# Optimization experiments

Measured on AMD Instinct MI355X. Metric: run time of the kernel, lower is better.

Reference implementation:

```python
import jax, jax.numpy as jnp
import numpy as np

NUM_SRC = 100000  # block src nodes
NUM_DST = 50000   # block dst nodes (first NUM_DST of src in DGL convention)
E = 800000        # edges, avg in-degree 16
D = 128           # in_dim == out_dim


def setup_inputs() -> dict:
    key = jax.random.key(0)
    k0, k1, k2, k3, k4 = jax.random.split(key, 5)
    h = jax.random.normal(k0, (NUM_SRC, D), dtype=jnp.float32)
    src = jax.random.randint(k1, (E,), 0, NUM_SRC)
    dst = jax.random.randint(k2, (E,), 0, NUM_DST)
    # GraphConv params: weight (in_dim, out_dim), bias (out_dim,)
    W = jax.random.normal(k3, (D, D), dtype=jnp.float32) / np.float32(np.sqrt(D))
    b = jnp.zeros((D,), dtype=jnp.float32)
    # gene_attn: Linear(out_dim, 1, bias=False)
    w_attn = jax.random.normal(k4, (D, 1), dtype=jnp.float32) / np.float32(np.sqrt(D))
    return {"h": h, "src": src, "dst": dst, "W": W, "b": b, "w_attn": w_attn}


def reference(h, src, dst, W, b, w_attn):
    ones = jnp.ones(src.shape, dtype=h.dtype)
    # DGL GraphConv norm='both': scale by out-degree(src)^-1/2 and in-degree(dst)^-1/2,
    # degrees clamped to min 1 (allow_zero_in_degree=True).
    deg_src = jax.ops.segment_sum(ones, src, num_segments=NUM_SRC)
    deg_dst = jax.ops.segment_sum(ones, dst, num_segments=NUM_DST)
    h_src = h * jax.lax.rsqrt(jnp.maximum(deg_src, 1.0))[:, None]
    # gather neighbor feats [E, D] then scatter-sum into dst nodes
    agg = jax.ops.segment_sum(h_src[src], dst, num_segments=NUM_DST)
    agg = agg * jax.lax.rsqrt(jnp.maximum(deg_dst, 1.0))[:, None]
    # in_dim == out_dim -> aggregate-then-weight (DGL order)
    out = agg @ W + b  # h[:num_dst] equivalent: agg is already dst-sized
    alpha = jax.nn.sigmoid(out @ w_attn)  # [NUM_DST, 1]
    return out * alpha, alpha
```

## Files before the change

kernel.cpp:

```cpp
#include <hip/hip_runtime.h>
#include <hip/hip_bf16.h>
#include <math.h>

#define DD 128
#define MAXDEG 64
#define BKT 64
#define SBKT 16
#define NB_MAX 1024
#define P_CH 8192
#define HBINS 16384
#define HBLK  32
#define HTHR  1024

using bf16x8 = __attribute__((ext_vector_type(8))) short;
using f32x4  = __attribute__((ext_vector_type(4))) float;

struct alignas(16) bfq { __hip_bfloat162 q[4]; };

__device__ inline float bf2f(short s) {
    unsigned int u = ((unsigned int)(unsigned short)s) << 16;
    float f;
    __builtin_memcpy(&f, &u, 4);
    return f;
}

__global__ __launch_bounds__(1024) void k1_kernel(
        const int* __restrict__ src, const int* __restrict__ dst,
        unsigned int* __restrict__ parts, unsigned int* __restrict__ bucket_cnt,
        int E, int NB, int nHist) {
    __shared__ unsigned int smem[HBINS];
    int t = threadIdx.x;
    int bid = blockIdx.x;
    if (bid < nHist) {
        int pass = bid / HBLK;
        int blk  = bid % HBLK;
        int lo   = pass * HBINS;
        for (int i = t; i < HBINS; i += 1024) smem[i] = 0;
        __syncthreads();
        int chunk = (E + HBLK - 1) / HBLK;
        int c0 = blk * chunk;
        int c1 = c0 + chunk; if (c1 > E) c1 = E;
        for (int i = c0 + t; i < c1; i += 1024) {
            unsigned int u = (unsigned int)(src[i] - lo);
            if (u < HBINS) atomicAdd(&smem[u], 1u);
        }
        __syncthreads();
        unsigned int* dstp = parts + ((size_t)bid << 14);
        for (int i = t; i < HBINS; i += 1024) dstp[i] = smem[i];
    } else {
        int b2 = bid - nHist;
        for (int b = t; b < NB; b += 1024) smem[b] = 0;
        __syncthreads();
        int c0 = b2 * P_CH;
        int c1 = c0 + P_CH; if (c1 > E) c1 = E;
        for (int i = c0 + t; i < c1; i += 1024)
            atomicAdd(&smem[dst[i] >> 6], 1u);
        __syncthreads();
        for (int b = t; b < NB; b += 1024)
            if (smem[b]) atomicAdd(&bucket_cnt[b], smem[b]);
    }
}

__global__ __launch_bounds__(256) void k2_kernel(
        const unsigned int* __restrict__ parts, unsigned int* __restrict__ deg_src,
        int num_src, const unsigned int* __restrict__ bucket_cnt,
        unsigned int* __restrict__ bucket_base, unsigned int* __restrict__ bucket_cur,
        int NB, int nMerge) {
    int bid = blockIdx.x;
    if (bid < nMerge) {
        int g = bid * 256 + threadIdx.x;
        if (g >= num_src) return;
        int pass = g >> 14;
        int r = g & (HBINS - 1);
        const unsigned int* p = parts + ((size_t)(pass * HBLK) << 14) + r;
        unsigned int s = 0;
#pragma unroll
        for (int b = 0; b < HBLK; ++b) s += p[(size_t)b << 14];
        deg_src[g] = s;
    } else {
        int lane = threadIdx.x;
        if (lane >= 64) return;
        unsigned int carry = 0;
        for (int b0 = 0; b0 < NB; b0 += 64) {
            int i = b0 + lane;
            unsigned int v = (i < NB) ? bucket_cnt[i] : 0u;
            unsigned int incl = v;
#pragma unroll
            for (int off = 1; off < 64; off <<= 1) {
                unsigned int u = __shfl_up(incl, off);
                if (lane >= off) incl += u;
            }
            unsigned int excl = incl - v + carry;
            if (i < NB) { bucket_base[i] = excl; bucket_cur[i] = excl; }
            carry += __shfl(incl, 63);
        }
        if (lane == 0) bucket_base[NB] = carry;
    }
}

__global__ __launch_bounds__(1024) void k3_kernel(
        const float* __restrict__ h, const unsigned int* __restrict__ deg_src,
        __hip_bfloat16* __restrict__ hb, const float* __restrict__ Wm,
        __hip_bfloat16* __restrict__ Wt, const int* __restrict__ src,
        const int* __restrict__ dst, unsigned int* __restrict__ bucket_cur,
        unsigned int* __restrict__ eparts, int E, int NB, int num_src,
        int nConv, int nWt) {
    __shared__ unsigned int smem[15360];
    int t = threadIdx.x;
    int bid = blockIdx.x;
    if (bid < nConv) {
        int idx = bid * 1024 + t;
        int total = num_src * (DD / 8);
        if (idx >= total) return;
        int row = idx >> 4;
        int c0  = (idx & 15) * 8;
        float nrm = rsqrtf(fmaxf((float)deg_src[row], 1.0f));
        const float4* p = reinterpret_cast<const float4*>(h + (size_t)row * DD + c0);
        float4 a = p[0], b = p[1];
        bfq o;
        o.q[0] = __float22bfloat162_rn(make_float2(a.x * nrm, a.y * nrm));
        o.q[1] = __float22bfloat162_rn(make_float2(a.z * nrm, a.w * nrm));
        o.q[2] = __float22bfloat162_rn(make_float2(b.x * nrm, b.y * nrm));
        o.q[3] = __float22bfloat162_rn(make_float2(b.z * nrm, b.w * nrm));
        *reinterpret_cast<bfq*>(hb + (size_t)row * DD + c0) = o;
    } else if (bid < nConv + nWt) {
        int idx = (bid - nConv) * 1024 + t;
        if (idx < DD * DD) {
            int c = idx >> 7, k = idx & 127;
            Wt[idx] = __float2bfloat16(Wm[k * DD + c]);
        }
    } else {
        int b2 = bid - nConv - nWt;
        unsigned int*   stage_s = smem;
        unsigned short* stage_d = (unsigned short*)(smem + 8192);
        unsigned int*   lhist   = smem + 12288;
        unsigned int*   lbase   = smem + 13312;
        unsigned int*   gbase   = smem + 14336;
        for (int b = t; b < NB_MAX; b += 1024) lhist[b] = 0;
        __syncthreads();
        int c0 = b2 * P_CH;
        int cnt = E - c0; if (cnt > P_CH) cnt = P_CH;
        int dreg[8], sreg[8];
#pragma unroll
        for (int k = 0; k < 8; ++k) {
            int j = t + k * 1024;
            if (j < cnt) {
                dreg[k] = dst[c0 + j];
                sreg[k] = src[c0 + j];
                atomicAdd(&lhist[dreg[k] >> 6], 1u);
            }
        }
        __syncthreads();
        int wid = t >> 6, lane = t & 63;
        unsigned int v = lhist[t];
        unsigned int x = v;
#pragma unroll
        for (int off = 1; off < 64; off <<= 1) {
            unsigned int u = __shfl_up(x, off);
            if (lane >= off) x += u;
        }
        if (lane == 63) gbase[wid] = x;
        __syncthreads();
        if (t < 16) {
            unsigned int w = gbase[t];
            unsigned int y = w;
#pragma unroll
            for (int off = 1; off < 16; off <<= 1) {
                unsigned int u = __shfl_up(y, off);
                if (t >= off) y += u;
            }
            gbase[t] = y - w;
        }
        __syncthreads();
        unsigned int excl = x - v + gbase[wid];
        __syncthreads();
        lbase[t] = excl;
        if (t < NB) {
            unsigned int c = lhist[t];
            gbase[t] = c ? atomicAdd(&bucket_cur[t], c) : 0u;
            lhist[t] = 0u;
        }
        __syncthreads();
#pragma unroll
        for (int k = 0; k < 8; ++k) {
            int j = t + k * 1024;
            if (j < cnt) {
                int bin = dreg[k] >> 6;
                unsigned int pos = lbase[bin] + atomicAdd(&lhist[bin], 1u);
                stage_d[pos] = (unsigned short)dreg[k];
                stage_s[pos] = (unsigned int)sreg[k];
            }
        }
        __syncthreads();
        for (int idx = t; idx < cnt; idx += 1024) {
            unsigned int d = stage_d[idx];
            unsigned int bin = d >> 6;
            unsigned int pos = gbase[bin] + ((unsigned int)idx - lbase[bin]);
            eparts[pos] = ((d & 63u) << 24) | stage_s[idx];
        }
    }
}

__global__ __launch_bounds__(256) void bgather_mfma_kernel(
        const __hip_bfloat16* __restrict__ hb,
        const unsigned int* __restrict__ eparts,
        const unsigned int* __restrict__ bucket_base,
        const __hip_bfloat16* __restrict__ Wt,
        const float* __restrict__ bias, const float* __restrict__ w_attn,
        float* __restrict__ out, float* __restrict__ alpha_out, int num_dst) {
    __shared__ unsigned int lcsr[SBKT * MAXDEG];
    __shared__ unsigned int cur[SBKT];
    __shared__ __hip_bfloat16 sagg[SBKT * DD];
    int t = threadIdx.x, wid = t >> 6, lane = t & 63;
    int b = blockIdx.x >> 2;
    unsigned int quarter = blockIdx.x & 3;
    if (t < SBKT) cur[t] = 0;
    __syncthreads();
    unsigned int e0 = bucket_base[b], e1 = bucket_base[b + 1];
    for (unsigned int i = e0 + t; i < e1; i += 256) {
        unsigned int e = eparts[i];
        unsigned int dlow = e >> 24;
        if ((dlow >> 4) == quarter) {
            unsigned int pos = atomicAdd(&cur[dlow & 15], 1u);
            if (pos < MAXDEG) lcsr[(dlow & 15) * MAXDEG + pos] = e & 0xFFFFFFu;
        }
    }
    __syncthreads();

    const bf16x8* hb8 = reinterpret_cast<const bf16x8*>(hb);
    char* sb = (char*)sagg;
    int g  = lane >> 4;
    int gl = lane & 15;
    {
        int r = wid * 4 + g;
        unsigned int degu = cur[r];
        int deg = (int)degu; if (deg > MAXDEG) deg = MAXDEG;
        const unsigned int* crow = &lcsr[r * MAXDEG];
        float acc[8];
#pragma unroll
        for (int j = 0; j < 8; ++j) acc[j] = 0.f;
        int i = 0;
        for (; i + 8 <= deg; i += 8) {
            uint4 qa = *reinterpret_cast<const uint4*>(crow + i);
            uint4 qb = *reinterpret_cast<const uint4*>(crow + i + 4);
            bf16x8 v0 = hb8[(size_t)qa.x * 16 + gl];
            bf16x8 v1 = hb8[(size_t)qa.y * 16 + gl];
            bf16x8 v2 = hb8[(size_t)qa.z * 16 + gl];
            bf16x8 v3 = hb8[(size_t)qa.w * 16 + gl];
            bf16x8 v4 = hb8[(size_t)qb.x * 16 + gl];
            bf16x8 v5 = hb8[(size_t)qb.y * 16 + gl];
            bf16x8 v6 = hb8[(size_t)qb.z * 16 + gl];
            bf16x8 v7 = hb8[(size_t)qb.w * 16 + gl];
#pragma unroll
            for (int j = 0; j < 8; ++j)
                acc[j] += ((bf2f(v0[j]) + bf2f(v1[j])) + (bf2f(v2[j]) + bf2f(v3[j])))
                        + ((bf2f(v4[j]) + bf2f(v5[j])) + (bf2f(v6[j]) + bf2f(v7[j])));
        }
        for (; i + 4 <= deg; i += 4) {
            uint4 q = *reinterpret_cast<const uint4*>(crow + i);
            bf16x8 v0 = hb8[(size_t)q.x * 16 + gl];
            bf16x8 v1 = hb8[(size_t)q.y * 16 + gl];
            bf16x8 v2 = hb8[(size_t)q.z * 16 + gl];
            bf16x8 v3 = hb8[(size_t)q.w * 16 + gl];
#pragma unroll
            for (int j = 0; j < 8; ++j)
                acc[j] += (bf2f(v0[j]) + bf2f(v1[j])) + (bf2f(v2[j]) + bf2f(v3[j]));
        }
        for (; i < deg; ++i) {
            bf16x8 v = hb8[(size_t)crow[i] * 16 + gl];
#pragma unroll
            for (int j = 0; j < 8; ++j) acc[j] += bf2f(v[j]);
        }
        float scd = rsqrtf(fmaxf((float)degu, 1.0f));
        bfq o;
#pragma unroll
        for (int j = 0; j < 4; ++j)
            o.q[j] = __float22bfloat162_rn(
                make_float2(acc[2 * j] * scd, acc[2 * j + 1] * scd));
        int byte = r * 256 + gl * 16;
        *reinterpret_cast<bfq*>(sb + (byte ^ ((r & 7) << 4))) = o;
    }
    __syncthreads();

    if (wid == 0) {
        int col = lane & 15, hi = lane >> 4;
        int row0 = b * 64 + quarter * 16;
        f32x4 acc[8];
#pragma unroll
        for (int ct = 0; ct < 8; ++ct) acc[ct] = (f32x4)0.f;
#pragma unroll
        for (int kg = 0; kg < 4; ++kg) {
            int byte = col * 256 + (kg * 32 + hi * 8) * 2;
            bf16x8 a = *reinterpret_cast<const bf16x8*>(
                sb + (byte ^ ((col & 7) << 4)));
#pragma unroll
            for (int ct = 0; ct < 8; ++ct) {
                const bf16x8* B = reinterpret_cast<const bf16x8*>(
                    Wt + (size_t)(ct * 16 + col) * DD);
                bf16x8 bb = B[kg * 4 + hi];
                acc[ct] = __builtin_amdgcn_mfma_f32_16x16x32_bf16(a, bb, acc[ct],
                                                                  0, 0, 0);
            }
        }
        float wv[8], bv[8];
#pragma unroll
        for (int ct = 0; ct < 8; ++ct) {
            wv[ct] = w_attn[ct * 16 + col];
            bv[ct] = bias[ct * 16 + col];
        }
#pragma unroll
        for (int r = 0; r < 4; ++r) {
            int row = row0 + hi * 4 + r;
            float v[8];
            float s = 0.f;
#pragma unroll
            for (int ct = 0; ct < 8; ++ct) {
                v[ct] = acc[ct][r] + bv[ct];
                s = fmaf(v[ct], wv[ct], s);
            }
            s += __shfl_xor(s, 1);
            s += __shfl_xor(s, 2);
            s += __shfl_xor(s, 4);
            s += __shfl_xor(s, 8);
            float alpha = 1.0f / (1.0f + expf(-s));
            if (row < num_dst) {
#pragma unroll
                for (int ct = 0; ct < 8; ++ct)
                    out[(size_t)row * DD + ct * 16 + col] = v[ct] * alpha;
                if (col == 0) alpha_out[row] = alpha;
            }
        }
    }
}

__global__ void hist_atomic_kernel(const int* __restrict__ src,
                                   unsigned int* __restrict__ deg_src, int E) {
    int i = blockIdx.x * blockDim.x + threadIdx.x;
    if (i < E) atomicAdd(&deg_src[src[i]], 1u);
}

__global__ void fillc_kernel(const int* __restrict__ src, const int* __restrict__ dst,
                             unsigned int* __restrict__ cursor,
                             int* __restrict__ csr, int E) {
    int i = blockIdx.x * blockDim.x + threadIdx.x;
    if (i < E) {
        int s = src[i];
        int d = dst[i];
        unsigned int pos = atomicAdd(&cursor[d], 1u);
        if (pos < MAXDEG) csr[(size_t)d * MAXDEG + pos] = s;
    }
}

__global__ __launch_bounds__(256) void gather_kernel(
        const __hip_bfloat16* __restrict__ hb,
        const int* __restrict__ csr, const unsigned int* __restrict__ cursor,
        __hip_bfloat16* __restrict__ aggb, int num_dst) {
    int wave = threadIdx.x >> 6;
    int lane = threadIdx.x & 63;
    int row = blockIdx.x * 4 + wave;
    if (row >= num_dst) return;
    unsigned int degu = cursor[row];
    int deg = (int)degu; if (deg > MAXDEG) deg = MAXDEG;
    const int* crow = csr + (size_t)row * MAXDEG;
    int c = lane * 2;
    float ax = 0.f, ay = 0.f;
    int i = 0;
    for (; i + 4 <= deg; i += 4) {
        int4 s0 = *reinterpret_cast<const int4*>(crow + i);
        float2 v0 = __bfloat1622float2(*reinterpret_cast<const __hip_bfloat162*>(hb + (size_t)s0.x * DD + c));
        float2 v1 = __bfloat1622float2(*reinterpret_cast<const __hip_bfloat162*>(hb + (size_t)s0.y * DD + c));
        float2 v2 = __bfloat1622float2(*reinterpret_cast<const __hip_bfloat162*>(hb + (size_t)s0.z * DD + c));
        float2 v3 = __bfloat1622float2(*reinterpret_cast<const __hip_bfloat162*>(hb + (size_t)s0.w * DD + c));
        ax += v0.x + v1.x + v2.x + v3.x;
        ay += v0.y + v1.y + v2.y + v3.y;
    }
    for (; i < deg; ++i) {
        int s = crow[i];
        float2 vv = __bfloat1622float2(*reinterpret_cast<const __hip_bfloat162*>(hb + (size_t)s * DD + c));
        ax += vv.x; ay += vv.y;
    }
    float scd = rsqrtf(fmaxf((float)degu, 1.0f));
    *reinterpret_cast<__hip_bfloat162*>(aggb + (size_t)row * DD + c) =
        __float22bfloat162_rn(make_float2(ax * scd, ay * scd));
}

__global__ __launch_bounds__(256) void out_mfma_kernel(
        const __hip_bfloat16* __restrict__ aggb,
        const __hip_bfloat16* __restrict__ Wt,
        const float* __restrict__ bias, const float* __restrict__ w_attn,
        float* __restrict__ out, float* __restrict__ alpha_out, int num_dst) {
    int wave = threadIdx.x >> 6;
    int lane = threadIdx.x & 63;
    int row0 = blockIdx.x * 64 + wave * 16;
    if (row0 >= num_dst) return;
    int col = lane & 15;
    int hi  = lane >> 4;
    int arow = row0 + col;
    if (arow >= num_dst) arow = num_dst - 1;
    f32x4 acc[8];
#pragma unroll
    for (int ct = 0; ct < 8; ++ct) acc[ct] = (f32x4)0.f;
    const bf16x8* A = reinterpret_cast<const bf16x8*>(aggb + (size_t)arow * DD);
#pragma unroll
    for (int kg = 0; kg < 4; ++kg) {
        bf16x8 a = A[kg * 4 + hi];
#pragma unroll
        for (int ct = 0; ct < 8; ++ct) {
            const bf16x8* B =
                reinterpret_cast<const bf16x8*>(Wt + (size_t)(ct * 16 + col) * DD);
            bf16x8 b = B[kg * 4 + hi];
            acc[ct] = __builtin_amdgcn_mfma_f32_16x16x32_bf16(a, b, acc[ct], 0, 0, 0);
        }
    }
    float wv[8], bv[8];
#pragma unroll
    for (int ct = 0; ct < 8; ++ct) {
        wv[ct] = w_attn[ct * 16 + col];
        bv[ct] = bias[ct * 16 + col];
    }
#pragma unroll
    for (int r = 0; r < 4; ++r) {
        int row = row0 + hi * 4 + r;
        float v[8];
        float s = 0.f;
#pragma unroll
        for (int ct = 0; ct < 8; ++ct) {
            v[ct] = acc[ct][r] + bv[ct];
            s = fmaf(v[ct], wv[ct], s);
        }
        s += __shfl_xor(s, 1);
        s += __shfl_xor(s, 2);
        s += __shfl_xor(s, 4);
        s += __shfl_xor(s, 8);
        float alpha = 1.0f / (1.0f + expf(-s));
        if (row < num_dst) {
#pragma unroll
            for (int ct = 0; ct < 8; ++ct)
                out[(size_t)row * DD + ct * 16 + col] = v[ct] * alpha;
            if (col == 0) alpha_out[row] = alpha;
        }
    }
}

extern "C" void kernel_launch(void* const* d_in, const int* in_sizes, int n_in,
                              void* d_out, int out_size, void* d_ws, size_t ws_size,
                              hipStream_t stream) {
    const float* h      = (const float*)d_in[0];
    const int*   src    = (const int*)d_in[1];
    const int*   dst    = (const int*)d_in[2];
    const float* Wm     = (const float*)d_in[3];
    const float* bias   = (const float*)d_in[4];
    const float* w_attn = (const float*)d_in[5];

    int num_src = in_sizes[0] / DD;
    int E       = in_sizes[1];
    int num_dst = out_size / (DD + 1);
    int NB      = (num_dst + BKT - 1) / BKT;
    int NPASS   = (num_src + HBINS - 1) / HBINS;

    float* out       = (float*)d_out;
    float* alpha_out = out + (size_t)num_dst * DD;

    char* p = (char*)d_ws;
    auto take = [&p](size_t bytes) {
        char* q = p;
        p += (bytes + 255) & ~(size_t)255;
        return q;
    };
    unsigned int* deg_src = (unsigned int*)take((size_t)num_src * 4);
    unsigned int* cursor  = (unsigned int*)take((size_t)num_dst * 4);
    int*          csr     = (int*)take((size_t)num_dst * MAXDEG * 4);
    __hip_bfloat16* aggb  = (__hip_bfloat16*)take((size_t)num_dst * DD * 2);
    __hip_bfloat16* Wt    = (__hip_bfloat16*)take((size_t)DD * DD * 2);
    __hip_bfloat16* hb    = (__hip_bfloat16*)take((size_t)num_src * DD * 2);
    unsigned int* parts   = (unsigned int*)take(((size_t)NPASS * HBLK) << 16);
    size_t full_need = (size_t)(p - (char*)d_ws);

    unsigned int* eparts      = (unsigned int*)csr;
    unsigned int* bucket_cnt  = eparts + ((E + 7) & ~7);
    unsigned int* bucket_base = bucket_cnt + NB + 8;
    unsigned int* bucket_cur  = bucket_base + NB + 8;

    bool use_mp = ws_size >= full_need;
    bool bucket_ok = use_mp && NB <= NB_MAX && num_dst <= 65536 &&
                     num_src < (1 << 24) &&
                     ((size_t)E + 3 * NB + 32) * 4 <= (size_t)num_dst * MAXDEG * 4;

    int thr = 256;
    int nHist  = NPASS * HBLK;
    int nPc    = (E + P_CH - 1) / P_CH;
    int nMerge = (num_src + 255) / 256;
    int nConv  = (num_src * (DD / 8) + 1023) / 1024;
    int nWt    = (DD * DD + 1023) / 1024;

    if (bucket_ok) {
        hipMemsetAsync(bucket_cnt, 0, (size_t)NB * 4, stream);
        k1_kernel<<<nHist + nPc, 1024, 0, stream>>>(src, dst, parts, bucket_cnt,
                                                    E, NB, nHist);
        k2_kernel<<<nMerge + 1, 256, 0, stream>>>(parts, deg_src, num_src,
                                                  bucket_cnt, bucket_base,
                                                  bucket_cur, NB, nMerge);
        k3_kernel<<<nConv + nWt + nPc, 1024, 0, stream>>>(
            h, deg_src, hb, Wm, Wt, src, dst, bucket_cur, eparts, E, NB, num_src,
            nConv, nWt);
        bgather_mfma_kernel<<<NB * 4, 256, 0, stream>>>(hb, eparts, bucket_base, Wt,
                                                        bias, w_attn, out, alpha_out,
                                                        num_dst);
    } else if (use_mp) {
        hipMemsetAsync(cursor, 0, (size_t)num_dst * 4, stream);
        k1_kernel<<<nHist, 1024, 0, stream>>>(src, dst, parts, cursor ,
                                              E, 0, nHist);
        k2_kernel<<<nMerge, 256, 0, stream>>>(parts, deg_src, num_src, cursor,
                                              cursor, cursor, 0, nMerge);
        fillc_kernel<<<(E + thr - 1) / thr, thr, 0, stream>>>(src, dst, cursor,
                                                              csr, E);
        k3_kernel<<<nConv + nWt, 1024, 0, stream>>>(
            h, deg_src, hb, Wm, Wt, src, dst, cursor, (unsigned int*)csr, E, 0,
            num_src, nConv, nWt);
        int grid_g = (num_dst + 3) / 4;
        gather_kernel<<<grid_g, thr, 0, stream>>>(hb, csr, cursor, aggb, num_dst);
        int grid_c = (num_dst + 63) / 64;
        out_mfma_kernel<<<grid_c, thr, 0, stream>>>(aggb, Wt, bias, w_attn,
                                                    out, alpha_out, num_dst);
    } else {
        hipMemsetAsync(deg_src, 0, (size_t)num_src * 4, stream);
        hipMemsetAsync(cursor, 0, (size_t)num_dst * 4, stream);
        hist_atomic_kernel<<<(E + thr - 1) / thr, thr, 0, stream>>>(src, deg_src, E);
        fillc_kernel<<<(E + thr - 1) / thr, thr, 0, stream>>>(src, dst, cursor,
                                                              csr, E);
        k3_kernel<<<nConv + nWt, 1024, 0, stream>>>(
            h, deg_src, hb, Wm, Wt, src, dst, cursor, (unsigned int*)csr, E, 0,
            num_src, nConv, nWt);
        int grid_g = (num_dst + 3) / 4;
        gather_kernel<<<grid_g, thr, 0, stream>>>(hb, csr, cursor, aggb, num_dst);
        int grid_c = (num_dst + 63) / 64;
        out_mfma_kernel<<<grid_c, thr, 0, stream>>>(aggb, Wt, bias, w_attn,
                                                    out, alpha_out, num_dst);
    }
}
```

Before: 95.25 us.

## Split epilogue GEMM across all four waves and remap blocks for XCD locality

The 16x128 output GEMM and epilogue used to run on wave 0 only. It is now split so each of the four waves computes two column tiles, with the attention dot product reduced across waves through shared-memory atomics and an extra barrier. Block indices are remapped so that consecutive work items land on the same XCD, which should improve L2 locality. Edge-list loads and output stores use nontemporal hints. The cost is extra synchronisation and shared atomics, and float atomic ordering makes the sum non-deterministic.

Result: slower. 98.05 us (+2.9%).

```diff
diff --git a/kernel.cpp b/kernel.cpp
--- a/kernel.cpp
+++ b/kernel.cpp
@@ -210,15 +210,22 @@
         float* __restrict__ out, float* __restrict__ alpha_out, int num_dst) {
     __shared__ unsigned int lcsr[SBKT * MAXDEG];
     __shared__ unsigned int cur[SBKT];
+    __shared__ float psum[SBKT];
     __shared__ __hip_bfloat16 sagg[SBKT * DD];
     int t = threadIdx.x, wid = t >> 6, lane = t & 63;
-    int b = blockIdx.x >> 2;
-    unsigned int quarter = blockIdx.x & 3;
+
+    int nwg = gridDim.x;
+    int q8 = nwg >> 3, r8 = nwg & 7;
+    int xcd = blockIdx.x & 7, pos8 = blockIdx.x >> 3;
+    int work = (xcd < r8 ? xcd * (q8 + 1) : r8 * (q8 + 1) + (xcd - r8) * q8) + pos8;
+    int b = work >> 2;
+    unsigned int quarter = work & 3;
+
     if (t < SBKT) cur[t] = 0;
     __syncthreads();
     unsigned int e0 = bucket_base[b], e1 = bucket_base[b + 1];
     for (unsigned int i = e0 + t; i < e1; i += 256) {
-        unsigned int e = eparts[i];
+        unsigned int e = __builtin_nontemporal_load(eparts + i);
         unsigned int dlow = e >> 24;
         if ((dlow >> 4) == quarter) {
             unsigned int pos = atomicAdd(&cur[dlow & 15], 1u);
@@ -281,53 +288,66 @@
         *reinterpret_cast<bfq*>(sb + (byte ^ ((r & 7) << 4))) = o;
     }
     __syncthreads();
-
-    if (wid == 0) {
+    if (t < SBKT) psum[t] = 0.f;
+    __syncthreads();
+
+    {
         int col = lane & 15, hi = lane >> 4;
         int row0 = b * 64 + quarter * 16;
-        f32x4 acc[8];
-#pragma unroll
-        for (int ct = 0; ct < 8; ++ct) acc[ct] = (f32x4)0.f;
+        f32x4 acc[2];
+        acc[0] = (f32x4)0.f;
+        acc[1] = (f32x4)0.f;
 #pragma unroll
         for (int kg = 0; kg < 4; ++kg) {
             int byte = col * 256 + (kg * 32 + hi * 8) * 2;
             bf16x8 a = *reinterpret_cast<const bf16x8*>(
                 sb + (byte ^ ((col & 7) << 4)));
 #pragma unroll
-            for (int ct = 0; ct < 8; ++ct) {
+            for (int c2 = 0; c2 < 2; ++c2) {
+                int ct = wid * 2 + c2;
                 const bf16x8* B = reinterpret_cast<const bf16x8*>(
                     Wt + (size_t)(ct * 16 + col) * DD);
                 bf16x8 bb = B[kg * 4 + hi];
-                acc[ct] = __builtin_amdgcn_mfma_f32_16x16x32_bf16(a, bb, acc[ct],
+                acc[c2] = __builtin_amdgcn_mfma_f32_16x16x32_bf16(a, bb, acc[c2],
                                                                   0, 0, 0);
             }
         }
-        float wv[8], bv[8];
-#pragma unroll
-        for (int ct = 0; ct < 8; ++ct) {
-            wv[ct] = w_attn[ct * 16 + col];
-            bv[ct] = bias[ct * 16 + col];
+        float wv[2], bv[2], v[2][4];
+#pragma unroll
+        for (int c2 = 0; c2 < 2; ++c2) {
+            int ct = wid * 2 + c2;
+            wv[c2] = w_attn[ct * 16 + col];
+            bv[c2] = bias[ct * 16 + col];
         }
 #pragma unroll
         for (int r = 0; r < 4; ++r) {
-            int row = row0 + hi * 4 + r;
-            float v[8];
             float s = 0.f;
 #pragma unroll
-            for (int ct = 0; ct < 8; ++ct) {
-                v[ct] = acc[ct][r] + bv[ct];
-                s = fmaf(v[ct], wv[ct], s);
+            for (int c2 = 0; c2 < 2; ++c2) {
+                v[c2][r] = acc[c2][r] + bv[c2];
+                s = fmaf(v[c2][r], wv[c2], s);
             }
             s += __shfl_xor(s, 1);
             s += __shfl_xor(s, 2);
             s += __shfl_xor(s, 4);
             s += __shfl_xor(s, 8);
-            float alpha = 1.0f / (1.0f + expf(-s));
+            if (col == 0) atomicAdd(&psum[hi * 4 + r], s);
+        }
+        __syncthreads();
+#pragma unroll
+        for (int r = 0; r < 4; ++r) {
+            int lrow = hi * 4 + r;
+            int row = row0 + lrow;
+            float alpha = 1.0f / (1.0f + expf(-psum[lrow]));
             if (row < num_dst) {
 #pragma unroll
-                for (int ct = 0; ct < 8; ++ct)
-                    out[(size_t)row * DD + ct * 16 + col] = v[ct] * alpha;
-                if (col == 0) alpha_out[row] = alpha;
+                for (int c2 = 0; c2 < 2; ++c2) {
+                    int ct = wid * 2 + c2;
+                    __builtin_nontemporal_store(
+                        v[c2][r] * alpha, &out[(size_t)row * DD + ct * 16 + col]);
+                }
+                if (wid == 0 && col == 0)
+                    __builtin_nontemporal_store(alpha, &alpha_out[row]);
             }
         }
     }
```

## Decouple bf16 conversion of h from source-degree norm and apply norm in gather

Applied to the files above, without the earlier changes.

The h-to-bf16 conversion and W transpose move into the first histogram kernel, so they no longer wait for source degrees and run alongside the histogram and bucket-count work. The per-source degree norm becomes a small float array, and the gather loops apply it to each neighbor row with FMAs. This shortens the dependent chain before the partition kernel. In exchange the gather does one extra scattered 4-byte load per edge and replaces the pairwise add tree with serial FMAs, which changes rounding slightly and lengthens the dependency chain.

After: 100.9 us. 1.06x slower.

```diff
diff --git a/kernel.cpp b/kernel.cpp
--- a/kernel.cpp
+++ b/kernel.cpp
@@ -10,7 +10,6 @@
 #define P_CH 8192
 #define HBINS 16384
 #define HBLK  32
-#define HTHR  1024
 
 using bf16x8 = __attribute__((ext_vector_type(8))) short;
 using f32x4  = __attribute__((ext_vector_type(4))) float;
@@ -25,15 +24,32 @@
 }
 
 __global__ __launch_bounds__(1024) void k1_kernel(
+        const float* __restrict__ h, __hip_bfloat16* __restrict__ hb,
         const int* __restrict__ src, const int* __restrict__ dst,
         unsigned int* __restrict__ parts, unsigned int* __restrict__ bucket_cnt,
-        int E, int NB, int nHist) {
+        const float* __restrict__ Wm, __hip_bfloat16* __restrict__ Wt,
+        int E, int NB, int num_src, int nConv, int nHist, int nPc) {
     __shared__ unsigned int smem[HBINS];
     int t = threadIdx.x;
     int bid = blockIdx.x;
-    if (bid < nHist) {
-        int pass = bid / HBLK;
-        int blk  = bid % HBLK;
+    if (bid < nConv) {
+        int idx = bid * 1024 + t;
+        int total = num_src * (DD / 8);
+        if (idx >= total) return;
+        int row = idx >> 4;
+        int c0  = (idx & 15) * 8;
+        const float4* p = reinterpret_cast<const float4*>(h + (size_t)row * DD + c0);
+        float4 a = p[0], b = p[1];
+        bfq o;
+        o.q[0] = __float22bfloat162_rn(make_float2(a.x, a.y));
+        o.q[1] = __float22bfloat162_rn(make_float2(a.z, a.w));
+        o.q[2] = __float22bfloat162_rn(make_float2(b.x, b.y));
+        o.q[3] = __float22bfloat162_rn(make_float2(b.z, b.w));
+        *reinterpret_cast<bfq*>(hb + (size_t)row * DD + c0) = o;
+    } else if (bid < nConv + nHist) {
+        int hbid = bid - nConv;
+        int pass = hbid / HBLK;
+        int blk  = hbid % HBLK;
         int lo   = pass * HBINS;
         for (int i = t; i < HBINS; i += 1024) smem[i] = 0;
         __syncthreads();
@@ -45,10 +61,10 @@
             if (u < HBINS) atomicAdd(&smem[u], 1u);
         }
         __syncthreads();
-        unsigned int* dstp = parts + ((size_t)bid << 14);
+        unsigned int* dstp = parts + ((size_t)hbid << 14);
         for (int i = t; i < HBINS; i += 1024) dstp[i] = smem[i];
-    } else {
-        int b2 = bid - nHist;
+    } else if (bid < nConv + nHist + nPc) {
+        int b2 = bid - nConv - nHist;
         for (int b = t; b < NB; b += 1024) smem[b] = 0;
         __syncthreads();
         int c0 = b2 * P_CH;
@@ -58,6 +74,12 @@
         __syncthreads();
         for (int b = t; b < NB; b += 1024)
             if (smem[b]) atomicAdd(&bucket_cnt[b], smem[b]);
+    } else {
+        int idx = (bid - nConv - nHist - nPc) * 1024 + t;
+        if (idx < DD * DD) {
+            int c = idx >> 7, k = idx & 127;
+            Wt[idx] = __float2bfloat16(Wm[k * DD + c]);
+        }
     }
 }
 
@@ -99,38 +121,18 @@
 }
 
 __global__ __launch_bounds__(1024) void k3_kernel(
-        const float* __restrict__ h, const unsigned int* __restrict__ deg_src,
-        __hip_bfloat16* __restrict__ hb, const float* __restrict__ Wm,
-        __hip_bfloat16* __restrict__ Wt, const int* __restrict__ src,
-        const int* __restrict__ dst, unsigned int* __restrict__ bucket_cur,
-        unsigned int* __restrict__ eparts, int E, int NB, int num_src,
-        int nConv, int nWt) {
+        const unsigned int* __restrict__ deg_src, float* __restrict__ norm_src,
+        const int* __restrict__ src, const int* __restrict__ dst,
+        unsigned int* __restrict__ bucket_cur, unsigned int* __restrict__ eparts,
+        int E, int NB, int num_src, int nNorm) {
     __shared__ unsigned int smem[15360];
     int t = threadIdx.x;
     int bid = blockIdx.x;
-    if (bid < nConv) {
-        int idx = bid * 1024 + t;
-        int total = num_src * (DD / 8);
-        if (idx >= total) return;
-        int row = idx >> 4;
-        int c0  = (idx & 15) * 8;
-        float nrm = rsqrtf(fmaxf((float)deg_src[row], 1.0f));
-        const float4* p = reinterpret_cast<const float4*>(h + (size_t)row * DD + c0);
-        float4 a = p[0], b = p[1];
-        bfq o;
-        o.q[0] = __float22bfloat162_rn(make_float2(a.x * nrm, a.y * nrm));
-        o.q[1] = __float22bfloat162_rn(make_float2(a.z * nrm, a.w * nrm));
-        o.q[2] = __float22bfloat162_rn(make_float2(b.x * nrm, b.y * nrm));
-        o.q[3] = __float22bfloat162_rn(make_float2(b.z * nrm, b.w * nrm));
-        *reinterpret_cast<bfq*>(hb + (size_t)row * DD + c0) = o;
-    } else if (bid < nConv + nWt) {
-        int idx = (bid - nConv) * 1024 + t;
-        if (idx < DD * DD) {
-            int c = idx >> 7, k = idx & 127;
-            Wt[idx] = __float2bfloat16(Wm[k * DD + c]);
-        }
+    if (bid < nNorm) {
+        int i = bid * 1024 + t;
+        if (i < num_src) norm_src[i] = rsqrtf(fmaxf((float)deg_src[i], 1.0f));
     } else {
-        int b2 = bid - nConv - nWt;
+        int b2 = bid - nNorm;
         unsigned int*   stage_s = smem;
         unsigned short* stage_d = (unsigned short*)(smem + 8192);
         unsigned int*   lhist   = smem + 12288;
@@ -203,6 +205,7 @@
 
 __global__ __launch_bounds__(256) void bgather_mfma_kernel(
         const __hip_bfloat16* __restrict__ hb,
+        const float* __restrict__ norm_src,
         const unsigned int* __restrict__ eparts,
         const unsigned int* __restrict__ bucket_base,
         const __hip_bfloat16* __restrict__ Wt,
@@ -243,6 +246,10 @@
         for (; i + 8 <= deg; i += 8) {
             uint4 qa = *reinterpret_cast<const uint4*>(crow + i);
             uint4 qb = *reinterpret_cast<const uint4*>(crow + i + 4);
+            float n0 = norm_src[qa.x], n1 = norm_src[qa.y];
+            float n2 = norm_src[qa.z], n3 = norm_src[qa.w];
+            float n4 = norm_src[qb.x], n5 = norm_src[qb.y];
+            float n6 = norm_src[qb.z], n7 = norm_src[qb.w];
             bf16x8 v0 = hb8[(size_t)qa.x * 16 + gl];
             bf16x8 v1 = hb8[(size_t)qa.y * 16 + gl];
             bf16x8 v2 = hb8[(size_t)qa.z * 16 + gl];
@@ -252,24 +259,39 @@
             bf16x8 v6 = hb8[(size_t)qb.z * 16 + gl];
             bf16x8 v7 = hb8[(size_t)qb.w * 16 + gl];
 #pragma unroll
-            for (int j = 0; j < 8; ++j)
-                acc[j] += ((bf2f(v0[j]) + bf2f(v1[j])) + (bf2f(v2[j]) + bf2f(v3[j])))
-                        + ((bf2f(v4[j]) + bf2f(v5[j])) + (bf2f(v6[j]) + bf2f(v7[j])));
+            for (int j = 0; j < 8; ++j) {
+                acc[j] = fmaf(bf2f(v0[j]), n0, acc[j]);
+                acc[j] = fmaf(bf2f(v1[j]), n1, acc[j]);
+                acc[j] = fmaf(bf2f(v2[j]), n2, acc[j]);
+                acc[j] = fmaf(bf2f(v3[j]), n3, acc[j]);
+                acc[j] = fmaf(bf2f(v4[j]), n4, acc[j]);
+                acc[j] = fmaf(bf2f(v5[j]), n5, acc[j]);
+                acc[j] = fmaf(bf2f(v6[j]), n6, acc[j]);
+                acc[j] = fmaf(bf2f(v7[j]), n7, acc[j]);
+            }
         }
         for (; i + 4 <= deg; i += 4) {
             uint4 q = *reinterpret_cast<const uint4*>(crow + i);
+            float n0 = norm_src[q.x], n1 = norm_src[q.y];
+            float n2 = norm_src[q.z], n3 = norm_src[q.w];
             bf16x8 v0 = hb8[(size_t)q.x * 16 + gl];
             bf16x8 v1 = hb8[(size_t)q.y * 16 + gl];
             bf16x8 v2 = hb8[(size_t)q.z * 16 + gl];
             bf16x8 v3 = hb8[(size_t)q.w * 16 + gl];
 #pragma unroll
-            for (int j = 0; j < 8; ++j)
-                acc[j] += (bf2f(v0[j]) + bf2f(v1[j])) + (bf2f(v2[j]) + bf2f(v3[j]));
+            for (int j = 0; j < 8; ++j) {
+                acc[j] = fmaf(bf2f(v0[j]), n0, acc[j]);
+                acc[j] = fmaf(bf2f(v1[j]), n1, acc[j]);
+                acc[j] = fmaf(bf2f(v2[j]), n2, acc[j]);
+                acc[j] = fmaf(bf2f(v3[j]), n3, acc[j]);
+            }
         }
         for (; i < deg; ++i) {
-            bf16x8 v = hb8[(size_t)crow[i] * 16 + gl];
-#pragma unroll
-            for (int j = 0; j < 8; ++j) acc[j] += bf2f(v[j]);
+            unsigned int s = crow[i];
+            float nn = norm_src[s];
+            bf16x8 v = hb8[(size_t)s * 16 + gl];
+#pragma unroll
+            for (int j = 0; j < 8; ++j) acc[j] = fmaf(bf2f(v[j]), nn, acc[j]);
         }
         float scd = rsqrtf(fmaxf((float)degu, 1.0f));
         bfq o;
@@ -352,7 +374,7 @@
 }
 
 __global__ __launch_bounds__(256) void gather_kernel(
-        const __hip_bfloat16* __restrict__ hb,
+        const __hip_bfloat16* __restrict__ hb, const float* __restrict__ norm_src,
         const int* __restrict__ csr, const unsigned int* __restrict__ cursor,
         __hip_bfloat16* __restrict__ aggb, int num_dst) {
     int wave = threadIdx.x >> 6;
@@ -367,17 +389,22 @@
     int i = 0;
     for (; i + 4 <= deg; i += 4) {
         int4 s0 = *reinterpret_cast<const int4*>(crow + i);
+        float n0 = norm_src[s0.x], n1 = norm_src[s0.y];
+        float n2 = norm_src[s0.z], n3 = norm_src[s0.w];
         float2 v0 = __bfloat1622float2(*reinterpret_cast<const __hip_bfloat162*>(hb + (size_t)s0.x * DD + c));
         float2 v1 = __bfloat1622float2(*reinterpret_cast<const __hip_bfloat162*>(hb + (size_t)s0.y * DD + c));
         float2 v2 = __bfloat1622float2(*reinterpret_cast<const __hip_bfloat162*>(hb + (size_t)s0.z * DD + c));
         float2 v3 = __bfloat1622float2(*reinterpret_cast<const __hip_bfloat162*>(hb + (size_t)s0.w * DD + c));
-        ax += v0.x + v1.x + v2.x + v3.x;
-        ay += v0.y + v1.y + v2.y + v3.y;
+        ax = fmaf(v0.x, n0, ax); ay = fmaf(v0.y, n0, ay);
+        ax = fmaf(v1.x, n1, ax); ay = fmaf(v1.y, n1, ay);
+        ax = fmaf(v2.x, n2, ax); ay = fmaf(v2.y, n2, ay);
+        ax = fmaf(v3.x, n3, ax); ay = fmaf(v3.y, n3, ay);
     }
     for (; i < deg; ++i) {
         int s = crow[i];
+        float nn = norm_src[s];
         float2 vv = __bfloat1622float2(*reinterpret_cast<const __hip_bfloat162*>(hb + (size_t)s * DD + c));
-        ax += vv.x; ay += vv.y;
+        ax = fmaf(vv.x, nn, ax); ay = fmaf(vv.y, nn, ay);
     }
     float scd = rsqrtf(fmaxf((float)degu, 1.0f));
     *reinterpret_cast<__hip_bfloat162*>(aggb + (size_t)row * DD + c) =
@@ -468,6 +495,7 @@
         return q;
     };
     unsigned int* deg_src = (unsigned int*)take((size_t)num_src * 4);
+    float*        norm_src= (float*)take((size_t)num_src * 4);
     unsigned int* cursor  = (unsigned int*)take((size_t)num_dst * 4);
     int*          csr     = (int*)take((size_t)num_dst * MAXDEG * 4);
     __hip_bfloat16* aggb  = (__hip_bfloat16*)take((size_t)num_dst * DD * 2);
@@ -492,33 +520,37 @@
     int nMerge = (num_src + 255) / 256;
     int nConv  = (num_src * (DD / 8) + 1023) / 1024;
     int nWt    = (DD * DD + 1023) / 1024;
+    int nNorm  = (num_src + 1023) / 1024;
 
     if (bucket_ok) {
         hipMemsetAsync(bucket_cnt, 0, (size_t)NB * 4, stream);
-        k1_kernel<<<nHist + nPc, 1024, 0, stream>>>(src, dst, parts, bucket_cnt,
-                                                    E, NB, nHist);
+        k1_kernel<<<nConv + nHist + nPc + nWt, 1024, 0, stream>>>(
+            h, hb, src, dst, parts, bucket_cnt, Wm, Wt, E, NB, num_src,
+            nConv, nHist, nPc);
         k2_kernel<<<nMerge + 1, 256, 0, stream>>>(parts, deg_src, num_src,
                                                   bucket_cnt, bucket_base,
                                                   bucket_cur, NB, nMerge);
-        k3_kernel<<<nConv + nWt + nPc, 1024, 0, stream>>>(
-            h, deg_src, hb, Wm, Wt, src, dst, bucket_cur, eparts, E, NB, num_src,
-            nConv, nWt);
-        bgather_mfma_kernel<<<NB * 4, 256, 0, stream>>>(hb, eparts, bucket_base, Wt,
-                                                        bias, w_attn, out, alpha_out,
-                                                        num_dst);
+        k3_kernel<<<nNorm + nPc, 1024, 0, stream>>>(deg_src, norm_src, src, dst,
+                                                    bucket_cur, eparts, E, NB,
+                                                    num_src, nNorm);
+        bgather_mfma_kernel<<<NB * 4, 256, 0, stream>>>(
+            hb, norm_src, eparts, bucket_base, Wt, bias, w_attn, out, alpha_out,
+            num_dst);
     } else if (use_mp) {
         hipMemsetAsync(cursor, 0, (size_t)num_dst * 4, stream);
-        k1_kernel<<<nHist, 1024, 0, stream>>>(src, dst, parts, cursor ,
-                                              E, 0, nHist);
+        k1_kernel<<<nConv + nHist + nWt, 1024, 0, stream>>>(
+            h, hb, src, dst, parts, bucket_cnt, Wm, Wt, E, 0, num_src,
+            nConv, nHist, 0);
         k2_kernel<<<nMerge, 256, 0, stream>>>(parts, deg_src, num_src, cursor,
                                               cursor, cursor, 0, nMerge);
+        k3_kernel<<<nNorm, 1024, 0, stream>>>(deg_src, norm_src, src, dst,
+                                              cursor, (unsigned int*)csr, E, 0,
+                                              num_src, nNorm);
         fillc_kernel<<<(E + thr - 1) / thr, thr, 0, stream>>>(src, dst, cursor,
                                                               csr, E);
-        k3_kernel<<<nConv + nWt, 1024, 0, stream>>>(
-            h, deg_src, hb, Wm, Wt, src, dst, cursor, (unsigned int*)csr, E, 0,
-            num_src, nConv, nWt);
         int grid_g = (num_dst + 3) / 4;
-        gather_kernel<<<grid_g, thr, 0, stream>>>(hb, csr, cursor, aggb, num_dst);
+        gather_kernel<<<grid_g, thr, 0, stream>>>(hb, norm_src, csr, cursor,
+                                                  aggb, num_dst);
         int grid_c = (num_dst + 63) / 64;
         out_mfma_kernel<<<grid_c, thr, 0, stream>>>(aggb, Wt, bias, w_attn,
                                                     out, alpha_out, num_dst);
@@ -526,13 +558,17 @@
         hipMemsetAsync(deg_src, 0, (size_t)num_src * 4, stream);
         hipMemsetAsync(cursor, 0, (size_t)num_dst * 4, stream);
         hist_atomic_kernel<<<(E + thr - 1) / thr, thr, 0, stream>>>(src, deg_src, E);
+        k1_kernel<<<nConv + nWt, 1024, 0, stream>>>(
+            h, hb, src, dst, parts, bucket_cnt, Wm, Wt, E, 0, num_src,
+            nConv, 0, 0);
+        k3_kernel<<<nNorm, 1024, 0, stream>>>(deg_src, norm_src, src, dst,
+                                              cursor, (unsigned int*)csr, E, 0,
+                                              num_src, nNorm);
         fillc_kernel<<<(E + thr - 1) / thr, thr, 0, stream>>>(src, dst, cursor,
                                                               csr, E);
-        k3_kernel<<<nConv + nWt, 1024, 0, stream>>>(
-            h, deg_src, hb, Wm, Wt, src, dst, cursor, (unsigned int*)csr, E, 0,
-            num_src, nConv, nWt);
         int grid_g = (num_dst + 3) / 4;
-        gather_kernel<<<grid_g, thr, 0, stream>>>(hb, csr, cursor, aggb, num_dst);
+        gather_kernel<<<grid_g, thr, 0, stream>>>(hb, norm_src, csr, cursor,
+                                                  aggb, num_dst);
         int grid_c = (num_dst + 63) / 64;
         out_mfma_kernel<<<grid_c, thr, 0, stream>>>(aggb, Wt, bias, w_attn,
                                                     out, alpha_out, num_dst);
```

## Move h fp32-to-bf16 conversion into histogram kernel, rescale in place later

Applied to the files above, without the earlier changes.

The bulk conversion of h to bf16, and the W transpose, move into the first kernel, so they run alongside the degree histogram and the bucket-count blocks. The degree normalisation is then applied by a separate in-place pass over the bf16 buffer in the third kernel. The aim is to fill idle compute units during the latency-bound histogram phase and take the large fp32 read off the critical path after the degree merge. In exchange, it adds an extra read and write of the full bf16 feature buffer and rounds to bf16 twice.

Result: slower. 101.4 us (+6.5%).

```diff
diff --git a/kernel.cpp b/kernel.cpp
--- a/kernel.cpp
+++ b/kernel.cpp
@@ -10,7 +10,6 @@
 #define P_CH 8192
 #define HBINS 16384
 #define HBLK  32
-#define HTHR  1024
 
 using bf16x8 = __attribute__((ext_vector_type(8))) short;
 using f32x4  = __attribute__((ext_vector_type(4))) float;
@@ -25,15 +24,32 @@
 }
 
 __global__ __launch_bounds__(1024) void k1_kernel(
+        const float* __restrict__ h, __hip_bfloat16* __restrict__ hb,
         const int* __restrict__ src, const int* __restrict__ dst,
         unsigned int* __restrict__ parts, unsigned int* __restrict__ bucket_cnt,
-        int E, int NB, int nHist) {
+        const float* __restrict__ Wm, __hip_bfloat16* __restrict__ Wt,
+        int E, int NB, int num_src, int nConv, int nHist, int nPc) {
     __shared__ unsigned int smem[HBINS];
     int t = threadIdx.x;
     int bid = blockIdx.x;
-    if (bid < nHist) {
-        int pass = bid / HBLK;
-        int blk  = bid % HBLK;
+    if (bid < nConv) {
+        int idx = bid * 1024 + t;
+        int total = num_src * (DD / 8);
+        if (idx >= total) return;
+        int row = idx >> 4;
+        int c0  = (idx & 15) * 8;
+        const float4* p = reinterpret_cast<const float4*>(h + (size_t)row * DD + c0);
+        float4 a = p[0], b = p[1];
+        bfq o;
+        o.q[0] = __float22bfloat162_rn(make_float2(a.x, a.y));
+        o.q[1] = __float22bfloat162_rn(make_float2(a.z, a.w));
+        o.q[2] = __float22bfloat162_rn(make_float2(b.x, b.y));
+        o.q[3] = __float22bfloat162_rn(make_float2(b.z, b.w));
+        *reinterpret_cast<bfq*>(hb + (size_t)row * DD + c0) = o;
+    } else if (bid < nConv + nHist) {
+        int hbid = bid - nConv;
+        int pass = hbid / HBLK;
+        int blk  = hbid % HBLK;
         int lo   = pass * HBINS;
         for (int i = t; i < HBINS; i += 1024) smem[i] = 0;
         __syncthreads();
@@ -45,10 +61,10 @@
             if (u < HBINS) atomicAdd(&smem[u], 1u);
         }
         __syncthreads();
-        unsigned int* dstp = parts + ((size_t)bid << 14);
+        unsigned int* dstp = parts + ((size_t)hbid << 14);
         for (int i = t; i < HBINS; i += 1024) dstp[i] = smem[i];
-    } else {
-        int b2 = bid - nHist;
+    } else if (bid < nConv + nHist + nPc) {
+        int b2 = bid - nConv - nHist;
         for (int b = t; b < NB; b += 1024) smem[b] = 0;
         __syncthreads();
         int c0 = b2 * P_CH;
@@ -58,6 +74,12 @@
         __syncthreads();
         for (int b = t; b < NB; b += 1024)
             if (smem[b]) atomicAdd(&bucket_cnt[b], smem[b]);
+    } else {
+        int idx = (bid - nConv - nHist - nPc) * 1024 + t;
+        if (idx < DD * DD) {
+            int c = idx >> 7, k = idx & 127;
+            Wt[idx] = __float2bfloat16(Wm[k * DD + c]);
+        }
     }
 }
 
@@ -99,38 +121,30 @@
 }
 
 __global__ __launch_bounds__(1024) void k3_kernel(
-        const float* __restrict__ h, const unsigned int* __restrict__ deg_src,
-        __hip_bfloat16* __restrict__ hb, const float* __restrict__ Wm,
-        __hip_bfloat16* __restrict__ Wt, const int* __restrict__ src,
-        const int* __restrict__ dst, unsigned int* __restrict__ bucket_cur,
-        unsigned int* __restrict__ eparts, int E, int NB, int num_src,
-        int nConv, int nWt) {
+        const unsigned int* __restrict__ deg_src, __hip_bfloat16* __restrict__ hb,
+        const int* __restrict__ src, const int* __restrict__ dst,
+        unsigned int* __restrict__ bucket_cur, unsigned int* __restrict__ eparts,
+        int E, int NB, int num_src, int nScale) {
     __shared__ unsigned int smem[15360];
     int t = threadIdx.x;
     int bid = blockIdx.x;
-    if (bid < nConv) {
+    if (bid < nScale) {
         int idx = bid * 1024 + t;
         int total = num_src * (DD / 8);
         if (idx >= total) return;
         int row = idx >> 4;
         int c0  = (idx & 15) * 8;
         float nrm = rsqrtf(fmaxf((float)deg_src[row], 1.0f));
-        const float4* p = reinterpret_cast<const float4*>(h + (size_t)row * DD + c0);
-        float4 a = p[0], b = p[1];
+        bfq v = *reinterpret_cast<const bfq*>(hb + (size_t)row * DD + c0);
         bfq o;
-        o.q[0] = __float22bfloat162_rn(make_float2(a.x * nrm, a.y * nrm));
-        o.q[1] = __float22bfloat162_rn(make_float2(a.z * nrm, a.w * nrm));
-        o.q[2] = __float22bfloat162_rn(make_float2(b.x * nrm, b.y * nrm));
-        o.q[3] = __float22bfloat162_rn(make_float2(b.z * nrm, b.w * nrm));
+#pragma unroll
+        for (int j = 0; j < 4; ++j) {
+            float2 f = __bfloat1622float2(v.q[j]);
+            o.q[j] = __float22bfloat162_rn(make_float2(f.x * nrm, f.y * nrm));
+        }
         *reinterpret_cast<bfq*>(hb + (size_t)row * DD + c0) = o;
-    } else if (bid < nConv + nWt) {
-        int idx = (bid - nConv) * 1024 + t;
-        if (idx < DD * DD) {
-            int c = idx >> 7, k = idx & 127;
-            Wt[idx] = __float2bfloat16(Wm[k * DD + c]);
-        }
     } else {
-        int b2 = bid - nConv - nWt;
+        int b2 = bid - nScale;
         unsigned int*   stage_s = smem;
         unsigned short* stage_d = (unsigned short*)(smem + 8192);
         unsigned int*   lhist   = smem + 12288;
@@ -495,28 +509,29 @@
 
     if (bucket_ok) {
         hipMemsetAsync(bucket_cnt, 0, (size_t)NB * 4, stream);
-        k1_kernel<<<nHist + nPc, 1024, 0, stream>>>(src, dst, parts, bucket_cnt,
-                                                    E, NB, nHist);
+        k1_kernel<<<nConv + nHist + nPc + nWt, 1024, 0, stream>>>(
+            h, hb, src, dst, parts, bucket_cnt, Wm, Wt, E, NB, num_src,
+            nConv, nHist, nPc);
         k2_kernel<<<nMerge + 1, 256, 0, stream>>>(parts, deg_src, num_src,
                                                   bucket_cnt, bucket_base,
                                                   bucket_cur, NB, nMerge);
-        k3_kernel<<<nConv + nWt + nPc, 1024, 0, stream>>>(
-            h, deg_src, hb, Wm, Wt, src, dst, bucket_cur, eparts, E, NB, num_src,
-            nConv, nWt);
-        bgather_mfma_kernel<<<NB * 4, 256, 0, stream>>>(hb, eparts, bucket_base, Wt,
-                                                        bias, w_attn, out, alpha_out,
-                                                        num_dst);
+        k3_kernel<<<nConv + nPc, 1024, 0, stream>>>(deg_src, hb, src, dst,
+                                                    bucket_cur, eparts, E, NB,
+                                                    num_src, nConv);
+        bgather_mfma_kernel<<<NB * 4, 256, 0, stream>>>(
+            hb, eparts, bucket_base, Wt, bias, w_attn, out, alpha_out, num_dst);
     } else if (use_mp) {
         hipMemsetAsync(cursor, 0, (size_t)num_dst * 4, stream);
-        k1_kernel<<<nHist, 1024, 0, stream>>>(src, dst, parts, cursor ,
-                                              E, 0, nHist);
+        k1_kernel<<<nConv + nHist + nWt, 1024, 0, stream>>>(
+            h, hb, src, dst, parts, bucket_cnt, Wm, Wt, E, 0, num_src,
+            nConv, nHist, 0);
         k2_kernel<<<nMerge, 256, 0, stream>>>(parts, deg_src, num_src, cursor,
                                               cursor, cursor, 0, nMerge);
+        k3_kernel<<<nConv, 1024, 0, stream>>>(deg_src, hb, src, dst,
+                                              cursor, (unsigned int*)csr, E, 0,
+                                              num_src, nConv);
         fillc_kernel<<<(E + thr - 1) / thr, thr, 0, stream>>>(src, dst, cursor,
                                                               csr, E);
-        k3_kernel<<<nConv + nWt, 1024, 0, stream>>>(
-            h, deg_src, hb, Wm, Wt, src, dst, cursor, (unsigned int*)csr, E, 0,
-            num_src, nConv, nWt);
         int grid_g = (num_dst + 3) / 4;
         gather_kernel<<<grid_g, thr, 0, stream>>>(hb, csr, cursor, aggb, num_dst);
         int grid_c = (num_dst + 63) / 64;
@@ -526,11 +541,14 @@
         hipMemsetAsync(deg_src, 0, (size_t)num_src * 4, stream);
         hipMemsetAsync(cursor, 0, (size_t)num_dst * 4, stream);
         hist_atomic_kernel<<<(E + thr - 1) / thr, thr, 0, stream>>>(src, deg_src, E);
+        k1_kernel<<<nConv + nWt, 1024, 0, stream>>>(
+            h, hb, src, dst, parts, bucket_cnt, Wm, Wt, E, 0, num_src,
+            nConv, 0, 0);
+        k3_kernel<<<nConv, 1024, 0, stream>>>(deg_src, hb, src, dst,
+                                              cursor, (unsigned int*)csr, E, 0,
+                                              num_src, nConv);
         fillc_kernel<<<(E + thr - 1) / thr, thr, 0, stream>>>(src, dst, cursor,
                                                               csr, E);
-        k3_kernel<<<nConv + nWt, 1024, 0, stream>>>(
-            h, deg_src, hb, Wm, Wt, src, dst, cursor, (unsigned int*)csr, E, 0,
-            num_src, nConv, nWt);
         int grid_g = (num_dst + 3) / 4;
         gather_kernel<<<grid_g, thr, 0, stream>>>(hb, csr, cursor, aggb, num_dst);
         int grid_c = (num_dst + 63) / 64;
```
